# Kernel optimization log

Hardware: AMD Instinct MI355X
Metric: run time of the kernel (lower is better)

The kernel has to match this reference:

```python
import jax, jax.numpy as jnp
import numpy as np
from jax import lax

B = 32768
INPUT_SIZE = 42  # 1 rocket_y + 20*(rock_x, rock_y) + 1 speed
H, W = 10, 15    # grid_height, grid_width
OUT = 3


def setup_inputs() -> dict:
    key = jax.random.key(0)
    ks = jax.random.split(key, 8)
    p = lambda k, s: (jax.random.normal(k, s) * 0.05).astype(jnp.float32)
    x = (jax.random.uniform(ks[0], (B, INPUT_SIZE)) * 16.0).astype(jnp.float32)
    return {
        "x": x,
        "conv1_w": p(ks[1], (16, 2, 3, 3)), "conv1_b": jnp.zeros((16,), jnp.float32),
        "conv2_w": p(ks[2], (32, 16, 3, 3)), "conv2_b": jnp.zeros((32,), jnp.float32),
        "fc1_w": p(ks[3], (32 * H * W + 1, 256)), "fc1_b": jnp.zeros((256,), jnp.float32),
        "fc2_w": p(ks[4], (256, 128)), "fc2_b": jnp.zeros((128,), jnp.float32),
        "fc3_w": p(ks[5], (128, OUT)), "fc3_b": jnp.zeros((OUT,), jnp.float32),
    }


def _conv(h, w, b):
    # 3x3, stride 1, padding 1 (SAME), NCHW / OIHW
    return lax.conv_general_dilated(h, w, (1, 1), "SAME",
                                    dimension_numbers=("NCHW", "OIHW", "NCHW")) \
           + b[None, :, None, None]


def _build_grid(x):
    """Vectorized replacement of the per-sample Python scatter loop."""
    bsz = x.shape[0]
    b = jnp.arange(bsz)
    dt = x.dtype
    # rocket channel: grid[i, rocket_y, 1] = 1 if 0 <= rocket_y < H
    ry = x[:, 0].astype(jnp.int32)
    rv = ((ry >= 0) & (ry < H)).astype(dt)
    rocket = jnp.zeros((bsz, H, W), dt).at[b, jnp.clip(ry, 0, H - 1), 1].add(rv)
    # rock channel: pairs (x, y) at columns (1,2),(3,4),...,(39,40)
    kx = x[:, 1:INPUT_SIZE - 1:2].astype(jnp.int32)  # [B, 20]
    ky = x[:, 2:INPUT_SIZE - 1:2].astype(jnp.int32)  # [B, 20]
    kv = ((kx >= 0) & (ky >= 0) & (kx < W) & (ky < H)).astype(dt)
    rock = jnp.zeros((bsz, H, W), dt).at[
        b[:, None], jnp.clip(ky, 0, H - 1), jnp.clip(kx, 0, W - 1)
    ].max(kv)  # set-to-1 semantics (duplicates ok)
    return jnp.stack([rocket, rock], axis=1)  # [B, 2, H, W]


def reference(x, conv1_w, conv1_b, conv2_w, conv2_b,
              fc1_w, fc1_b, fc2_w, fc2_b, fc3_w, fc3_b):
    grid = _build_grid(x)
    h = jax.nn.relu(_conv(grid, conv1_w, conv1_b))
    h = jax.nn.relu(_conv(h, conv2_w, conv2_b))
    h = h.reshape(x.shape[0], -1)                      # NCHW flatten, matches torch .view
    h = jnp.concatenate([h, x[:, -1:]], axis=1)        # append speed
    h = jax.nn.relu(h @ fc1_w + fc1_b)
    h = jax.nn.relu(h @ fc2_w + fc2_b)
    return h @ fc3_w + fc3_b
```

## Files before the change

kernel.cpp:

```cpp
#include <hip/hip_runtime.h>
#include <hip/hip_bf16.h>
#include <stdint.h>

typedef short short8 __attribute__((ext_vector_type(8)));
typedef float f32x4  __attribute__((ext_vector_type(4)));

__device__ __forceinline__ uint16_t f2bf(float f) {
    union { float f; uint32_t u; } v; v.f = f;
    return (uint16_t)((v.u + 0x7FFFu + ((v.u >> 16) & 1u)) >> 16);
}
__device__ __forceinline__ float bf2f(uint16_t h) {
    union { uint32_t u; float f; } v; v.u = ((uint32_t)h) << 16;
    return v.f;
}
__device__ __forceinline__ uint32_t pk2bf(float a, float b) {
    uint32_t r;
    asm("v_cvt_pk_bf16_f32 %0, %1, %2" : "=v"(r) : "v"(a), "v"(b));
    return r;
}
__device__ __forceinline__ void gl_lds16(const void* g, void* l) {
    __builtin_amdgcn_global_load_lds(
        (const __attribute__((address_space(1))) unsigned int*)g,
        (__attribute__((address_space(3))) unsigned int*)l, 16, 0, 0);
}

#define NSAMP_TOT 32768
#define H2_PER_S  5120

__global__ void repack_all(const float* __restrict__ f1w, const float* __restrict__ c2w,
                           const float* __restrict__ c1w, const float* __restrict__ f2w,
                           uint16_t* __restrict__ w1pt, uint16_t* __restrict__ w2rt,
                           uint16_t* __restrict__ w1rt, uint16_t* __restrict__ w2bt) {
    int tid = threadIdx.x, b = blockIdx.x;
    if (b < 160) {
        int f_s = b >> 4, cp = b & 15, n = tid;
        __align__(16) uint16_t vals[32];
        #pragma unroll
        for (int o = 0; o < 32; o++) {
            int c = cp * 2 + (o >> 4), pl = o & 15;
            int p = f_s * 16 + pl;
            float v = (p < 150) ? f1w[(size_t)(c * 150 + p) * 256 + n] : 0.f;
            vals[o] = f2bf(v);
        }
        int win = f_s * 8 + (cp >> 1);
        size_t rowbase = (size_t)n * H2_PER_S + win * 64;
        #pragma unroll
        for (int j = 0; j < 4; j++) {
            int qlog = (cp * 4 + j) & 7;
            int qphy = qlog ^ (n & 7);
            *(uint4*)&w1pt[rowbase + qphy * 8] = *(uint4*)&vals[j * 8];
        }
    } else if (b == 160) {
        for (int t = tid; t < 32 * 160; t += 256) {
            int n = t / 160, k = t % 160;
            float v = 0.f;
            if (k < 144) {
                int tap = k >> 4, ci = k & 15, dy = tap / 3, dx = tap % 3;
                v = c2w[((n * 16 + ci) * 3 + dy) * 3 + dx];
            }
            w2rt[t] = f2bf(v);
        }
        for (int t = tid; t < 16 * 32; t += 256) {
            int n = t >> 5, k = t & 31;
            float v = 0.f;
            if (k < 18) {
                int tap = k >> 1, ch = k & 1;
                int dy = (tap * 11) >> 5, dx = tap - dy * 3;
                v = c1w[((n * 2 + ch) * 3 + dy) * 3 + dx];
            }
            w1rt[t] = f2bf(v);
        }
    } else {
        __shared__ float tr2[32][129];
        int kb = b - 161;
        for (int i = tid; i < 32 * 128; i += 256) {
            int kk = i >> 7, n = i & 127;
            tr2[kk][n] = f2w[(size_t)(kb * 32 + kk) * 128 + n];
        }
        __syncthreads();
        int n = tid >> 1, half = tid & 1;
        __align__(16) uint16_t tmp[16];
        #pragma unroll
        for (int q = 0; q < 16; q++) tmp[q] = f2bf(tr2[half * 16 + q][n]);
        *(uint4*)&w2bt[(size_t)n * 256 + kb * 32 + half * 16]     = *(uint4*)&tmp[0];
        *(uint4*)&w2bt[(size_t)n * 256 + kb * 32 + half * 16 + 8] = *(uint4*)&tmp[8];
    }
}

__launch_bounds__(512, 2)
__global__ void k12_fused(const float* __restrict__ x, const uint16_t* __restrict__ w1rt,
                          const float* __restrict__ c1b, const uint16_t* __restrict__ w2rt,
                          const float* __restrict__ c2b, uint16_t* __restrict__ h2, int s0) {
    __shared__ float sx[8 * 42];
    __shared__ __align__(16) uint16_t grd[8 * 204 * 2];
    __shared__ __align__(16) uint16_t h1s[8 * 205 * 16];
    __shared__ uint16_t lutPO[160];
    __shared__ uint16_t lutST[160];
    int tid = threadIdx.x;
    int w = tid >> 6, l = tid & 63, lr = l & 15, lk = l >> 4;

    short8 b1f = *(const short8*)&w1rt[lr * 32 + lk * 8];
    short8 bfr[5][2];
    #pragma unroll
    for (int ks = 0; ks < 5; ks++)
        #pragma unroll
        for (int nf = 0; nf < 2; nf++)
            bfr[ks][nf] = *(const short8*)&w2rt[(nf * 16 + lr) * 160 + ks * 32 + lk * 8];
    float cb1r = c1b[lr];
    float cb0 = c2b[lr], cb1 = c2b[16 + lr];

    uint4 z4 = make_uint4(0, 0, 0, 0);
    for (int idx = tid; idx < 3688; idx += 512) {
        if (idx < 408) ((uint4*)grd)[idx] = z4;
        else           ((uint4*)h1s)[idx - 408] = z4;
    }
    int sbase = s0 + blockIdx.x * 8;
    if (tid < 336) sx[tid] = x[(size_t)(sbase + tid / 42) * 42 + (tid % 42)];
    if (tid >= 336 && tid < 496) {
        int p = tid - 336;
        int y = p / 15, xx = p - y * 15;
        int po = y * 17 + xx;
        lutPO[p] = (p < 150) ? (uint16_t)po : 0;
        lutST[p] = (p < 150) ? (uint16_t)((po + 18) * 16) : (uint16_t)(204 * 16);
    }
    __syncthreads();

    if (tid < 160) {
        int sl = tid / 20, r = tid % 20;
        int kx = (int)sx[sl * 42 + 1 + 2 * r];
        int ky = (int)sx[sl * 42 + 2 + 2 * r];
        if (kx >= 0 && kx < 15 && ky >= 0 && ky < 10)
            grd[(sl * 204 + (ky + 1) * 17 + (kx + 1)) * 2 + 1] = 0x3F80;
    } else if (tid < 168) {
        int sl = tid - 160;
        int ry = (int)sx[sl * 42];
        if (ry >= 0 && ry < 10)
            grd[(sl * 204 + (ry + 1) * 17 + 2) * 2 + 0] = 0x3F80;
    }
    __syncthreads();

    int goff[4]; uint32_t gmask[4];
    #pragma unroll
    for (int jj = 0; jj < 4; jj++) {
        int t = lk * 4 + jj;
        int tc = t < 9 ? t : 0;
        int dy = (tc * 11) >> 5, dx = tc - dy * 3;
        goff[jj] = dy * 17 + dx;
        gmask[jj] = (t < 9) ? 0xFFFFFFFFu : 0u;
    }
    int sbg  = w * 204;
    int sb16 = w * 205 * 16;

    #pragma unroll
    for (int f_s = 0; f_s < 10; f_s++) {
        int p160 = f_s * 16 + lr;
        int gbase = sbg + lutPO[p160];
        union { uint32_t d[4]; short8 s; } au;
        #pragma unroll
        for (int jj = 0; jj < 4; jj++) {
            uint32_t v = *(const uint32_t*)&grd[(gbase + goff[jj]) * 2];
            au.d[jj] = v & gmask[jj];
        }
        f32x4 acc = {};
        acc = __builtin_amdgcn_mfma_f32_16x16x32_bf16(au.s, b1f, acc, 0, 0, 0);
        #pragma unroll
        for (int j = 0; j < 4; j += 2) {
            float v0 = fmaxf(acc[j] + cb1r, 0.f);
            float v1 = fmaxf(acc[j + 1] + cb1r, 0.f);
            uint32_t pk = pk2bf(v0, v1);
            int p2 = f_s * 16 + lk * 4 + j;
            h1s[sb16 + lutST[p2] + lr]     = (uint16_t)pk;
            h1s[sb16 + lutST[p2 + 1] + lr] = (uint16_t)(pk >> 16);
        }
    }
    __syncthreads();

    int cdofs[5];
    #pragma unroll
    for (int ks = 0; ks < 5; ks++) {
        int idx = ks * 4 + lk;
        int idc = idx < 18 ? idx : 0;
        int tap = idc >> 1, half = idc & 1;
        int dy = (tap * 11) >> 5, dx = tap - dy * 3;
        cdofs[ks] = (dy * 17 + dx) * 16 + half * 8;
    }
    uint32_t kmask4 = ((16 + lk) < 18) ? 0xFFFFFFFFu : 0u;
    int k0lo = lr * 16 + lk * 4;
    int k0s_base = (k0lo & ~63) | ((((k0lo >> 3) & 7) ^ w) << 3) | (k0lo & 7);
    size_t sbh2 = (size_t)(blockIdx.x * 8 + w) * H2_PER_S;

    #pragma unroll
    for (int f_s = 0; f_s < 10; f_s++) {
        int p160 = f_s * 16 + lr;
        int abase = sb16 + lutPO[p160] * 16;
        f32x4 acc0 = {}, acc1 = {};
        #pragma unroll
        for (int ks = 0; ks < 5; ks++) {
            short8 av = *(const short8*)&h1s[abase + cdofs[ks]];
            if (ks == 4) {
                union { short8 s; uint32_t d[4]; } u; u.s = av;
                #pragma unroll
                for (int dd = 0; dd < 4; dd++) u.d[dd] &= kmask4;
                av = u.s;
            }
            acc0 = __builtin_amdgcn_mfma_f32_16x16x32_bf16(av, bfr[ks][0], acc0, 0, 0, 0);
            acc1 = __builtin_amdgcn_mfma_f32_16x16x32_bf16(av, bfr[ks][1], acc1, 0, 0, 0);
        }
        uint32_t p01 = pk2bf(fmaxf(acc0[0] + cb0, 0.f), fmaxf(acc0[1] + cb0, 0.f));
        uint32_t p23 = pk2bf(fmaxf(acc0[2] + cb0, 0.f), fmaxf(acc0[3] + cb0, 0.f));
        uint32_t q01 = pk2bf(fmaxf(acc1[0] + cb1, 0.f), fmaxf(acc1[1] + cb1, 0.f));
        uint32_t q23 = pk2bf(fmaxf(acc1[2] + cb1, 0.f), fmaxf(acc1[3] + cb1, 0.f));
        int k0s = f_s * 512 + k0s_base;
        *(uint2*)&h2[sbh2 + k0s]       = make_uint2(p01, p23);
        *(uint2*)&h2[sbh2 + k0s + 256] = make_uint2(q01, q23);
    }
}

__launch_bounds__(512)
__global__ void k3_fused(const uint16_t* __restrict__ h2, const uint16_t* __restrict__ w1pt,
                         const float* __restrict__ f1b, const float* __restrict__ f1w,
                         const float* __restrict__ x, const uint16_t* __restrict__ w2bt,
                         const float* __restrict__ f2b, const float* __restrict__ f3w,
                         const float* __restrict__ f3b, float* __restrict__ out, int s0) {
    #define BUF_E (64 * 64 + 256 * 64)
    __shared__ __align__(16) uint16_t uLDS[2 * BUF_E];
    uint16_t* lH = uLDS;
    __shared__ float sbias[256], swl[256], sspeed[64], sb2[128], sw3[384];
    __shared__ float pf[4][64][3];
    int tid = threadIdx.x;
    int bm = blockIdx.x;
    if (tid < 256) { sbias[tid] = f1b[tid]; swl[tid] = f1w[(size_t)4800 * 256 + tid]; }
    else if (tid < 320) sspeed[tid - 256] = x[(size_t)(s0 + bm * 64 + (tid - 256)) * 42 + 41];
    else if (tid < 448) sb2[tid - 320] = f2b[tid - 320];
    for (int i = tid; i < 384; i += 512) sw3[i] = f3w[i];

    int w = tid >> 6, l = tid & 63, lr = l & 15, lk = l >> 4;
    int wm = w >> 2, wn = w & 3;
    const uint16_t* ga = &h2[(size_t)(bm * 64 + (tid >> 3)) * H2_PER_S + (tid & 7) * 8];
    const uint16_t* gb[4];
    #pragma unroll
    for (int i = 0; i < 4; i++) {
        int c2 = tid + i * 512;
        gb[i] = &w1pt[(size_t)(c2 >> 3) * H2_PER_S + (c2 & 7) * 8];
    }
    int saOff = tid * 8;
    int sbOff[4];
    #pragma unroll
    for (int i = 0; i < 4; i++) sbOff[i] = 4096 + (tid + i * 512) * 8;
    int aoff[2][2], boff[4][2];
    #pragma unroll
    for (int ks = 0; ks < 2; ks++) {
        int cl = (ks * 4 + lk);
        #pragma unroll
        for (int mf = 0; mf < 2; mf++)
            aoff[mf][ks] = (wm * 32 + mf * 16 + lr) * 64 + ((cl ^ (lr & 7)) << 3);
        #pragma unroll
        for (int nf = 0; nf < 4; nf++)
            boff[nf][ks] = 4096 + (wn * 64 + nf * 16 + lr) * 64 + ((cl ^ (lr & 7)) << 3);
    }

    f32x4 acc[2][4] = {};
    gl_lds16(ga, uLDS + saOff); ga += 64;
    #pragma unroll
    for (int i = 0; i < 4; i++) { gl_lds16(gb[i], uLDS + sbOff[i]); gb[i] += 64; }
    __syncthreads();
    for (int kt = 0; kt < 80; kt++) {
        int cur = kt & 1;
        uint16_t* nbuf = uLDS + (cur ^ 1) * BUF_E;
        if (kt < 79) {
            gl_lds16(ga, nbuf + saOff); ga += 64;
            #pragma unroll
            for (int i = 0; i < 4; i++) { gl_lds16(gb[i], nbuf + sbOff[i]); gb[i] += 64; }
        }
        const uint16_t* buf = uLDS + cur * BUF_E;
        #pragma unroll
        for (int ks = 0; ks < 2; ks++) {
            short8 a[2], b[4];
            #pragma unroll
            for (int mf = 0; mf < 2; mf++)
                a[mf] = *(const short8*)&buf[aoff[mf][ks]];
            #pragma unroll
            for (int nf = 0; nf < 4; nf++)
                b[nf] = *(const short8*)&buf[boff[nf][ks]];
            #pragma unroll
            for (int mf = 0; mf < 2; mf++)
                #pragma unroll
                for (int nf = 0; nf < 4; nf++)
                    acc[mf][nf] = __builtin_amdgcn_mfma_f32_16x16x32_bf16(a[mf], b[nf], acc[mf][nf], 0, 0, 0);
        }
        __syncthreads();
    }
    #pragma unroll
    for (int mf = 0; mf < 2; mf++) {
        #pragma unroll
        for (int j = 0; j < 4; j++) {
            int r = wm * 32 + mf * 16 + lk * 4 + j;
            float sp = sspeed[r];
            #pragma unroll
            for (int nf = 0; nf < 4; nf++) {
                int col = wn * 64 + nf * 16 + lr;
                float v = acc[mf][nf][j] + sbias[col] + sp * swl[col];
                int cc = col >> 3, cl = col & 7;
                lH[r * 256 + ((cc ^ (r & 7)) << 3) + cl] = f2bf(v > 0.f ? v : 0.f);
            }
        }
    }
    __syncthreads();
    f32x4 acc2[2][2] = {};
    #pragma unroll
    for (int ks2 = 0; ks2 < 8; ks2++) {
        short8 a2[2], bv[2];
        #pragma unroll
        for (int mf2 = 0; mf2 < 2; mf2++) {
            int row = wm * 32 + mf2 * 16 + lr;
            int chunk = (ks2 * 4 + lk) ^ (row & 7);
            a2[mf2] = *(const short8*)&lH[row * 256 + chunk * 8];
        }
        #pragma unroll
        for (int nf2 = 0; nf2 < 2; nf2++)
            bv[nf2] = *(const short8*)&w2bt[(size_t)(wn * 32 + nf2 * 16 + lr) * 256 + ks2 * 32 + lk * 8];
        #pragma unroll
        for (int mf2 = 0; mf2 < 2; mf2++)
            #pragma unroll
            for (int nf2 = 0; nf2 < 2; nf2++)
                acc2[mf2][nf2] = __builtin_amdgcn_mfma_f32_16x16x32_bf16(a2[mf2], bv[nf2], acc2[mf2][nf2], 0, 0, 0);
    }
    float p3[2][4][3];
    #pragma unroll
    for (int mf2 = 0; mf2 < 2; mf2++)
        #pragma unroll
        for (int j = 0; j < 4; j++)
            #pragma unroll
            for (int o = 0; o < 3; o++) p3[mf2][j][o] = 0.f;
    #pragma unroll
    for (int mf2 = 0; mf2 < 2; mf2++) {
        #pragma unroll
        for (int nf2 = 0; nf2 < 2; nf2++) {
            int col = wn * 32 + nf2 * 16 + lr;
            float w0 = sw3[col * 3 + 0], w1v = sw3[col * 3 + 1], w2v = sw3[col * 3 + 2];
            #pragma unroll
            for (int j = 0; j < 4; j++) {
                float v = acc2[mf2][nf2][j] + sb2[col];
                v = v > 0.f ? v : 0.f;
                p3[mf2][j][0] += v * w0;
                p3[mf2][j][1] += v * w1v;
                p3[mf2][j][2] += v * w2v;
            }
        }
    }
    #pragma unroll
    for (int off = 1; off < 16; off <<= 1)
        #pragma unroll
        for (int mf2 = 0; mf2 < 2; mf2++)
            #pragma unroll
            for (int j = 0; j < 4; j++)
                #pragma unroll
                for (int o = 0; o < 3; o++)
                    p3[mf2][j][o] += __shfl_xor(p3[mf2][j][o], off);
    if (lr == 0) {
        #pragma unroll
        for (int mf2 = 0; mf2 < 2; mf2++)
            #pragma unroll
            for (int j = 0; j < 4; j++) {
                int r = wm * 32 + mf2 * 16 + lk * 4 + j;
                #pragma unroll
                for (int o = 0; o < 3; o++) pf[wn][r][o] = p3[mf2][j][o];
            }
    }
    __syncthreads();
    if (tid < 192) {
        int r = tid / 3, o = tid - r * 3;
        out[(size_t)(s0 + bm * 64 + r) * 3 + o] =
            pf[0][r][o] + pf[1][r][o] + pf[2][r][o] + pf[3][r][o] + f3b[o];
    }
    #undef BUF_E
}

extern "C" void kernel_launch(void* const* d_in, const int* in_sizes, int n_in,
                              void* d_out, int out_size, void* d_ws, size_t ws_size,
                              hipStream_t stream) {
    const float* x   = (const float*)d_in[0];
    const float* c1w = (const float*)d_in[1];
    const float* c1b = (const float*)d_in[2];
    const float* c2w = (const float*)d_in[3];
    const float* c2b = (const float*)d_in[4];
    const float* f1w = (const float*)d_in[5];
    const float* f1b = (const float*)d_in[6];
    const float* f2w = (const float*)d_in[7];
    const float* f2b = (const float*)d_in[8];
    const float* f3w = (const float*)d_in[9];
    const float* f3b = (const float*)d_in[10];
    float* out = (float*)d_out;

    char* ws = (char*)d_ws;
    uint16_t* w1pt = (uint16_t*)ws;
    uint16_t* w2rt = (uint16_t*)(ws + 2621440);
    uint16_t* w2bt = (uint16_t*)(ws + 2631680);
    uint16_t* w1rt = (uint16_t*)(ws + 2697216);
    size_t base = 2698240;

    int chunk = NSAMP_TOT;
    while (chunk > 128 && base + (size_t)chunk * 10240 > ws_size) chunk >>= 1;
    uint16_t* h2 = (uint16_t*)(ws + base);

    repack_all<<<169, 256, 0, stream>>>(f1w, c2w, c1w, f2w, w1pt, w2rt, w1rt, w2bt);

    for (int s0 = 0; s0 < NSAMP_TOT; s0 += chunk) {
        k12_fused<<<chunk / 8, 512, 0, stream>>>(x, w1rt, c1b, w2rt, c2b, h2, s0);
        k3_fused<<<chunk / 64, 512, 0, stream>>>(h2, w1pt, f1b, f1w, x, w2bt, f2b, f3w, f3b, out, s0);
    }
}
```

Baseline: 264.2 us.

## Load fc1 weight fragments directly into registers and stage only activations in LDS

The fc1 GEMM in k3_fused no longer stages the 256x64 weight tile through LDS each k-step. Each wave now owns a 32-column slice of N across all 64 rows and loads its B fragments straight from global memory into registers, double-buffered in registers. Only the A (activation) tile goes through LDS, double-buffered in two fixed halves with a manually unrolled two-step loop. This cuts LDS footprint and traffic, which may allow higher occupancy, but each wave now issues uncoalesced per-lane global loads for weights and relies on L2 reuse across blocks.

```diff
diff --git a/kernel.cpp b/kernel.cpp
--- a/kernel.cpp
+++ b/kernel.cpp
@@ -222,9 +222,10 @@
                          const float* __restrict__ x, const uint16_t* __restrict__ w2bt,
                          const float* __restrict__ f2b, const float* __restrict__ f3w,
                          const float* __restrict__ f3b, float* __restrict__ out, int s0) {
-    #define BUF_E (64 * 64 + 256 * 64)
-    __shared__ __align__(16) uint16_t uLDS[2 * BUF_E];
-    uint16_t* lH = uLDS;
+    __shared__ __align__(16) uint16_t uLDS[64 * 256];
+    uint16_t* lA0 = uLDS;
+    uint16_t* lA1 = uLDS + 4096;
+    uint16_t* lH  = uLDS;
     __shared__ float sbias[256], swl[256], sspeed[64], sb2[128], sw3[384];
     __shared__ float pf[4][64][3];
     int tid = threadIdx.x;
@@ -237,68 +238,75 @@
     int w = tid >> 6, l = tid & 63, lr = l & 15, lk = l >> 4;
     int wm = w >> 2, wn = w & 3;
     const uint16_t* ga = &h2[(size_t)(bm * 64 + (tid >> 3)) * H2_PER_S + (tid & 7) * 8];
-    const uint16_t* gb[4];
-    #pragma unroll
-    for (int i = 0; i < 4; i++) {
-        int c2 = tid + i * 512;
-        gb[i] = &w1pt[(size_t)(c2 >> 3) * H2_PER_S + (c2 & 7) * 8];
-    }
     int saOff = tid * 8;
-    int sbOff[4];
-    #pragma unroll
-    for (int i = 0; i < 4; i++) sbOff[i] = 4096 + (tid + i * 512) * 8;
-    int aoff[2][2], boff[4][2];
+    const uint16_t* gB[2][2];
+    #pragma unroll
+    for (int nf = 0; nf < 2; nf++)
+        #pragma unroll
+        for (int ks = 0; ks < 2; ks++) {
+            int n = w * 32 + nf * 16 + lr;
+            int cl = (ks * 4 + lk) ^ (lr & 7);
+            gB[nf][ks] = w1pt + (size_t)n * H2_PER_S + cl * 8;
+        }
+    int aoff[4][2];
     #pragma unroll
     for (int ks = 0; ks < 2; ks++) {
         int cl = (ks * 4 + lk);
         #pragma unroll
-        for (int mf = 0; mf < 2; mf++)
-            aoff[mf][ks] = (wm * 32 + mf * 16 + lr) * 64 + ((cl ^ (lr & 7)) << 3);
-        #pragma unroll
-        for (int nf = 0; nf < 4; nf++)
-            boff[nf][ks] = 4096 + (wn * 64 + nf * 16 + lr) * 64 + ((cl ^ (lr & 7)) << 3);
-    }
-
-    f32x4 acc[2][4] = {};
-    gl_lds16(ga, uLDS + saOff); ga += 64;
-    #pragma unroll
-    for (int i = 0; i < 4; i++) { gl_lds16(gb[i], uLDS + sbOff[i]); gb[i] += 64; }
-    __syncthreads();
-    for (int kt = 0; kt < 80; kt++) {
-        int cur = kt & 1;
-        uint16_t* nbuf = uLDS + (cur ^ 1) * BUF_E;
-        if (kt < 79) {
-            gl_lds16(ga, nbuf + saOff); ga += 64;
-            #pragma unroll
-            for (int i = 0; i < 4; i++) { gl_lds16(gb[i], nbuf + sbOff[i]); gb[i] += 64; }
-        }
-        const uint16_t* buf = uLDS + cur * BUF_E;
-        #pragma unroll
-        for (int ks = 0; ks < 2; ks++) {
-            short8 a[2], b[4];
-            #pragma unroll
-            for (int mf = 0; mf < 2; mf++)
-                a[mf] = *(const short8*)&buf[aoff[mf][ks]];
-            #pragma unroll
-            for (int nf = 0; nf < 4; nf++)
-                b[nf] = *(const short8*)&buf[boff[nf][ks]];
-            #pragma unroll
-            for (int mf = 0; mf < 2; mf++)
+        for (int mf = 0; mf < 4; mf++)
+            aoff[mf][ks] = (mf * 16 + lr) * 64 + ((cl ^ (lr & 7)) << 3);
+    }
+
+    f32x4 acc[4][2] = {};
+    short8 b0[2][2], b1[2][2];
+    gl_lds16(ga, lA0 + saOff); ga += 64;
+    #pragma unroll
+    for (int nf = 0; nf < 2; nf++)
+        #pragma unroll
+        for (int ks = 0; ks < 2; ks++) { b0[nf][ks] = *(const short8*)gB[nf][ks]; gB[nf][ks] += 64; }
+    __syncthreads();
+
+    #define K3_COMPUTE(LA, BB)                                                              \
+        _Pragma("unroll")                                                                   \
+        for (int ks = 0; ks < 2; ks++) {                                                    \
+            short8 a[4];                                                                    \
+            _Pragma("unroll")                                                               \
+            for (int mf = 0; mf < 4; mf++) a[mf] = *(const short8*)&(LA)[aoff[mf][ks]];     \
+            _Pragma("unroll")                                                               \
+            for (int mf = 0; mf < 4; mf++)                                                  \
+                _Pragma("unroll")                                                           \
+                for (int nf = 0; nf < 2; nf++)                                              \
+                    acc[mf][nf] = __builtin_amdgcn_mfma_f32_16x16x32_bf16(a[mf], (BB)[nf][ks], acc[mf][nf], 0, 0, 0); \
+        }
+
+    for (int kt2 = 0; kt2 < 40; kt2++) {
+        gl_lds16(ga, lA1 + saOff); ga += 64;
+        #pragma unroll
+        for (int nf = 0; nf < 2; nf++)
+            #pragma unroll
+            for (int ks = 0; ks < 2; ks++) { b1[nf][ks] = *(const short8*)gB[nf][ks]; gB[nf][ks] += 64; }
+        K3_COMPUTE(lA0, b0);
+        __syncthreads();
+        if (kt2 < 39) {
+            gl_lds16(ga, lA0 + saOff); ga += 64;
+            #pragma unroll
+            for (int nf = 0; nf < 2; nf++)
                 #pragma unroll
-                for (int nf = 0; nf < 4; nf++)
-                    acc[mf][nf] = __builtin_amdgcn_mfma_f32_16x16x32_bf16(a[mf], b[nf], acc[mf][nf], 0, 0, 0);
-        }
+                for (int ks = 0; ks < 2; ks++) { b0[nf][ks] = *(const short8*)gB[nf][ks]; gB[nf][ks] += 64; }
+        }
+        K3_COMPUTE(lA1, b1);
         __syncthreads();
     }
-    #pragma unroll
-    for (int mf = 0; mf < 2; mf++) {
+    #undef K3_COMPUTE
+    #pragma unroll
+    for (int mf = 0; mf < 4; mf++) {
         #pragma unroll
         for (int j = 0; j < 4; j++) {
-            int r = wm * 32 + mf * 16 + lk * 4 + j;
+            int r = mf * 16 + lk * 4 + j;
             float sp = sspeed[r];
             #pragma unroll
-            for (int nf = 0; nf < 4; nf++) {
-                int col = wn * 64 + nf * 16 + lr;
+            for (int nf = 0; nf < 2; nf++) {
+                int col = w * 32 + nf * 16 + lr;
                 float v = acc[mf][nf][j] + sbias[col] + sp * swl[col];
                 int cc = col >> 3, cl = col & 7;
                 lH[r * 256 + ((cc ^ (r & 7)) << 3) + cl] = f2bf(v > 0.f ? v : 0.f);
@@ -373,7 +381,6 @@
         out[(size_t)(s0 + bm * 64 + r) * 3 + o] =
             pf[0][r][o] + pf[1][r][o] + pf[2][r][o] + pf[3][r][o] + f3b[o];
     }
-    #undef BUF_E
 }
 
 extern "C" void kernel_launch(void* const* d_in, const int* in_sizes, int n_in,
```

Result: slower. 271.0 us (+2.6%).
